# Kernel tuning notes

Hardware: AMD Instinct MI355X
Metric: run time of the kernel (lower is better)

## Reference

```python
import jax, jax.numpy as jnp
import numpy as np

HEADS = 8
KEY_DIM = 32
EPS = 1e-5


def layernorm(x, gamma, beta, eps=EPS):
    mu = jnp.mean(x, axis=-1, keepdims=True)
    var = jnp.mean(jnp.square(x - mu), axis=-1, keepdims=True)
    return (x - mu) * jax.lax.rsqrt(var + eps) * gamma + beta


def setup_inputs() -> dict:
    key = jax.random.key(0)
    ks = jax.random.split(key, 6)
    B, H, W, C = 16, 32, 32, 256
    inner = HEADS * KEY_DIM  # 256
    s = 1.0 / np.sqrt(C)
    return {
        "x": jax.random.normal(ks[0], (B, H, W, C), jnp.float32),
        "gamma": jnp.ones((C,), jnp.float32),
        "beta": jnp.zeros((C,), jnp.float32),
        "Wq": jax.random.normal(ks[1], (C, inner), jnp.float32) * s,
        "bq": jnp.zeros((inner,), jnp.float32),
        "Wk": jax.random.normal(ks[2], (C, inner), jnp.float32) * s,
        "bk": jnp.zeros((inner,), jnp.float32),
        "Wv": jax.random.normal(ks[3], (C, inner), jnp.float32) * s,
        "bv": jnp.zeros((inner,), jnp.float32),
        "Wp": jax.random.normal(ks[4], (inner, C), jnp.float32) * s,
        "bp": jnp.zeros((C,), jnp.float32),
    }


def reference(x, gamma, beta, Wq, bq, Wk, bk, Wv, bv, Wp, bp):
    B, H, W, C = x.shape
    N = H * W
    h, d = HEADS, KEY_DIM
    X = layernorm(x, gamma, beta)              # [B,H,W,C]
    Xf = X.reshape(B, N, C)                    # 1x1 conv == per-token linear
    Q = (Xf @ Wq + bq).reshape(B, N, h, d)
    K = (Xf @ Wk + bk).reshape(B, N, h, d)
    V = (Xf @ Wv + bv).reshape(B, N, h, d)
    scale = jnp.asarray(d, x.dtype) ** -0.5
    scores = jnp.einsum('bnhd,bmhd->bhnm', Q, K) * scale
    A = jax.nn.softmax(scores, axis=-1)        # [B,h,N,N]
    Y = jnp.einsum('bhnm,bmhd->bnhd', A, V).reshape(B, N, h * d)
    out = (Y @ Wp + bp).reshape(B, H, W, C)
    return out
```

## Files before the change

### kernel.cpp

```cpp
#include <hip/hip_runtime.h>
#include <hip/hip_bf16.h>

typedef __bf16 bf16_t;
typedef __attribute__((ext_vector_type(8))) __bf16 bf16x8;
typedef __attribute__((ext_vector_type(4))) float f32x4;
typedef __attribute__((ext_vector_type(4))) short s16x4;

#define GLDS16(g, l) __builtin_amdgcn_global_load_lds( \
    (const __attribute__((address_space(1))) unsigned int*)(g), \
    (__attribute__((address_space(3))) unsigned int*)(l), 16, 0, 0)

__device__ __forceinline__ float fexp2(float x) {
#if __has_builtin(__builtin_amdgcn_exp2f)
  return __builtin_amdgcn_exp2f(x);
#else
  return exp2f(x);
#endif
}

#define QSCALE (0.17677669529663688f * 1.4426950408889634f)

__global__ __launch_bounds__(256) void wtr_kernel(
    const float* __restrict__ Wq, const float* __restrict__ Wk,
    const float* __restrict__ Wv, const float* __restrict__ Wp,
    bf16_t* __restrict__ Wt)
{
  const int idx = blockIdx.x * 256 + threadIdx.x;
  const int mat = idx >> 16;
  const int e   = idx & 65535;
  const int k   = e >> 8;
  const int n   = e & 255;
  const float* W = (mat == 0) ? Wq : (mat == 1) ? Wk : (mat == 2) ? Wv : Wp;
  Wt[(size_t)mat * 65536 + n * 256 + k] = (bf16_t)W[e];
}

__global__ __launch_bounds__(256) void ln_kernel(
    const float* __restrict__ x, const float* __restrict__ gamma,
    const float* __restrict__ beta, bf16_t* __restrict__ Xln)
{
  const int wave = threadIdx.x >> 6, lane = threadIdx.x & 63;
  const int tok = blockIdx.x * 4 + wave;
  const float4 v = *reinterpret_cast<const float4*>(x + (size_t)tok * 256 + lane * 4);
  float s1 = v.x + v.y + v.z + v.w;
  float s2 = v.x*v.x + v.y*v.y + v.z*v.z + v.w*v.w;
  #pragma unroll
  for (int off = 1; off < 64; off <<= 1) {
    s1 += __shfl_xor(s1, off);
    s2 += __shfl_xor(s2, off);
  }
  const float mean = s1 * (1.0f/256.0f);
  const float var  = s2 * (1.0f/256.0f) - mean*mean;
  const float rstd = rsqrtf(var + 1e-5f);
  const float4 g  = *reinterpret_cast<const float4*>(gamma + lane*4);
  const float4 be = *reinterpret_cast<const float4*>(beta  + lane*4);
  union { bf16_t h4[4]; unsigned long long u; } pk;
  pk.h4[0] = (bf16_t)((v.x-mean)*rstd*g.x + be.x);
  pk.h4[1] = (bf16_t)((v.y-mean)*rstd*g.y + be.y);
  pk.h4[2] = (bf16_t)((v.z-mean)*rstd*g.z + be.z);
  pk.h4[3] = (bf16_t)((v.w-mean)*rstd*g.w + be.w);
  *reinterpret_cast<unsigned long long*>(Xln + (size_t)tok*256 + lane*4) = pk.u;
}

template<int MODE>
__global__ __launch_bounds__(256) void gemm_kernel(
    const bf16_t* __restrict__ A, const bf16_t* __restrict__ Wt,
    const float* __restrict__ b0, const float* __restrict__ b1,
    const float* __restrict__ b2,
    bf16_t* __restrict__ Qb, bf16_t* __restrict__ Kb, bf16_t* __restrict__ Vt,
    float* __restrict__ Fout)
{
  __shared__ __align__(16) bf16_t As[128*64];
  __shared__ __align__(16) bf16_t Bs[128*64];
  const int tid  = threadIdx.x;
  const int lane = tid & 63, wave = tid >> 6;
  const int lg = lane >> 4, li = lane & 15;
  const int wm = wave >> 1, wn = wave & 1;
  const int mt = blockIdx.x;
  const int nt = blockIdx.y;
  int mat, nbase;
  const bf16_t* Bm;
  if (MODE == 0) { mat = nt >> 1; nbase = (nt & 1) * 128; Bm = Wt + (size_t)mat * 65536; }
  else           { mat = 3;       nbase = nt * 128;       Bm = Wt; }

  f32x4 acc[4][4] = {};

  for (int kt = 0; kt < 4; ++kt) {
    __syncthreads();
    #pragma unroll
    for (int i = 0; i < 4; ++i) {
      const int idx = i*256 + tid;
      const int row = idx >> 3, ck = idx & 7;
      const int cs = ck ^ (row & 7);
      GLDS16(A + (size_t)(mt*128 + row)*256 + kt*64 + cs*8, As + idx*8);
    }
    #pragma unroll
    for (int i = 0; i < 4; ++i) {
      const int idx = i*256 + tid;
      const int row = idx >> 3, ck = idx & 7;
      const int cs = ck ^ (row & 7);
      GLDS16(Bm + (size_t)(nbase + row)*256 + kt*64 + cs*8, Bs + idx*8);
    }
    __syncthreads();
    #pragma unroll
    for (int kk = 0; kk < 2; ++kk) {
      bf16x8 af[4], bfv[4];
      #pragma unroll
      for (int mi = 0; mi < 4; ++mi) {
        const int row = wm*64 + mi*16 + li;
        const int c = (kk*4 + lg) ^ (row & 7);
        af[mi] = *reinterpret_cast<const bf16x8*>(As + row*64 + c*8);
      }
      #pragma unroll
      for (int ni = 0; ni < 4; ++ni) {
        const int row = wn*64 + ni*16 + li;
        const int c = (kk*4 + lg) ^ (row & 7);
        bfv[ni] = *reinterpret_cast<const bf16x8*>(Bs + row*64 + c*8);
      }
      #pragma unroll
      for (int mi = 0; mi < 4; ++mi)
        #pragma unroll
        for (int ni = 0; ni < 4; ++ni)
          acc[mi][ni] = __builtin_amdgcn_mfma_f32_16x16x32_bf16(af[mi], bfv[ni], acc[mi][ni], 0, 0, 0);
    }
  }

  if (MODE == 0) {
    const float* bias = (mat == 0) ? b0 : (mat == 1) ? b1 : b2;
    if (mat < 2) {
      bf16_t* Out = (mat == 0) ? Qb : Kb;
      const float osc = (mat == 0) ? QSCALE : 1.0f;
      #pragma unroll
      for (int mi = 0; mi < 4; ++mi)
        #pragma unroll
        for (int ni = 0; ni < 4; ++ni) {
          const int col = nbase + wn*64 + ni*16 + li;
          const float bb = bias[col];
          #pragma unroll
          for (int r = 0; r < 4; ++r) {
            const int row = mt*128 + wm*64 + mi*16 + lg*4 + r;
            Out[(size_t)row*256 + col] = (bf16_t)((acc[mi][ni][r] + bb) * osc);
          }
        }
    } else {
      #pragma unroll
      for (int mi = 0; mi < 4; ++mi)
        #pragma unroll
        for (int ni = 0; ni < 4; ++ni) {
          const int col = nbase + wn*64 + ni*16 + li;
          const int hh = col >> 5, dd = col & 31;
          const float bb = bias[col];
          const int row0 = mt*128 + wm*64 + mi*16 + lg*4;
          const int bi = row0 >> 10, nn = row0 & 1023;
          union { bf16_t h4[4]; unsigned long long u; } pk;
          #pragma unroll
          for (int r = 0; r < 4; ++r) pk.h4[r] = (bf16_t)(acc[mi][ni][r] + bb);
          *reinterpret_cast<unsigned long long*>(
              Vt + ((size_t)(bi*8 + hh)*32 + dd)*1024 + nn) = pk.u;
        }
    }
  } else {
    #pragma unroll
    for (int mi = 0; mi < 4; ++mi)
      #pragma unroll
      for (int ni = 0; ni < 4; ++ni) {
        const int col = nbase + wn*64 + ni*16 + li;
        const float bb = b0[col];
        #pragma unroll
        for (int r = 0; r < 4; ++r) {
          const int row = mt*128 + wm*64 + mi*16 + lg*4 + r;
          Fout[(size_t)row*256 + col] = acc[mi][ni][r] + bb;
        }
      }
  }
}

__global__ __launch_bounds__(256, 4) void attn_kernel(
    const bf16_t* __restrict__ Qb, const bf16_t* __restrict__ Kb,
    const bf16_t* __restrict__ Vt, bf16_t* __restrict__ Yb)
{
  __shared__ __align__(16) char Ks[2][4096];
  __shared__ __align__(16) char Vs[2][4096];
  const int tid  = threadIdx.x;
  const int wave = tid >> 6, lane = tid & 63;
  const int lg = lane >> 4, li = lane & 15;
  const int gid = blockIdx.x;
  const int qt = (gid >> 3) & 7;
  const int bh = ((gid >> 6) << 3) | (gid & 7);
  const int b  = bh >> 3, hh = bh & 7;
  const int tok0 = b*1024 + qt*128 + wave*32;

  const bf16x8 qf0 = *reinterpret_cast<const bf16x8*>(
      Qb + (size_t)(tok0 + li)*256 + hh*32 + lg*8);
  const bf16x8 qf1 = *reinterpret_cast<const bf16x8*>(
      Qb + (size_t)(tok0 + 16 + li)*256 + hh*32 + lg*8);

  const int kt_ = tid >> 2, ks_ = tid & 3;
  const bf16_t* Ksrc = Kb + (size_t)(b*1024 + kt_)*256 + hh*32
                          + ((ks_ ^ ((kt_ >> 1) & 3)) * 8);
  const int vd_ = tid >> 3, vs_ = tid & 7;
  const bf16_t* Vsrc = Vt + ((size_t)bh*32 + vd_)*1024
                          + ((vs_ ^ (vd_ & 7)) * 8);

  const int kof = li*64 + ((lg ^ ((li >> 1) & 3)) * 16);
  int vof[4];
  #pragma unroll
  for (int ct = 0; ct < 4; ++ct)
    vof[ct] = li*128 + (((ct*2 + (lg >> 1)) ^ (li & 7)) * 16) + (lg & 1)*8;

  const f32x4 fz = {0.f, 0.f, 0.f, 0.f};
  f32x4 acc00 = fz, acc01 = fz;
  f32x4 acc10 = fz, acc11 = fz;
  float m0 = 0.f, m1 = 0.f;
  float lrow0 = 0.f, lrow1 = 0.f;

  GLDS16(Ksrc, &Ks[0][tid*16]);
  GLDS16(Vsrc, &Vs[0][tid*16]);
  __syncthreads();

  #pragma unroll 2
  for (int mc = 0; mc < 16; ++mc) {
    const int cur = mc & 1;
    if (mc < 15) {
      GLDS16(Ksrc + (size_t)(mc+1)*16384, &Ks[cur^1][tid*16]);
      GLDS16(Vsrc + (mc+1)*64,            &Vs[cur^1][tid*16]);
    }
    const char* kb = &Ks[cur][0];
    const char* vb = &Vs[cur][0];
    f32x4 s0[4], s1[4];
    #pragma unroll
    for (int ct = 0; ct < 4; ++ct) {
      const bf16x8 kfrag = *reinterpret_cast<const bf16x8*>(kb + kof + ct*1024);
      s0[ct] = __builtin_amdgcn_mfma_f32_16x16x32_bf16(kfrag, qf0, fz, 0, 0, 0);
      s1[ct] = __builtin_amdgcn_mfma_f32_16x16x32_bf16(kfrag, qf1, fz, 0, 0, 0);
    }
    s16x4 vq0[4], vq1[4];
    #pragma unroll
    for (int ct = 0; ct < 4; ++ct) {
      vq0[ct] = *reinterpret_cast<const s16x4*>(vb + vof[ct]);
      vq1[ct] = *reinterpret_cast<const s16x4*>(vb + vof[ct] + 16*128);
    }
    {
      float mxa = fmaxf(fmaxf(s0[0][0], s0[0][1]), fmaxf(s0[0][2], s0[0][3]));
      float mxb = fmaxf(fmaxf(s0[1][0], s0[1][1]), fmaxf(s0[1][2], s0[1][3]));
      float mxc = fmaxf(fmaxf(s0[2][0], s0[2][1]), fmaxf(s0[2][2], s0[2][3]));
      float mxd = fmaxf(fmaxf(s0[3][0], s0[3][1]), fmaxf(s0[3][2], s0[3][3]));
      const float pmax = fmaxf(fmaxf(mxa, mxb), fmaxf(mxc, mxd));
      if (!__all(pmax - m0 <= 8.0f)) {
        float rmx = pmax;
        rmx = fmaxf(rmx, __shfl_xor(rmx, 16));
        rmx = fmaxf(rmx, __shfl_xor(rmx, 32));
        const float mnew = fmaxf(m0, rmx);
        const float sf = fexp2(m0 - mnew);
        lrow0 *= sf;
        #pragma unroll
        for (int r = 0; r < 4; ++r) { acc00[r] *= sf; acc01[r] *= sf; }
        m0 = mnew;
      }
      float psum = 0.f;
      #pragma unroll
      for (int ct = 0; ct < 4; ++ct) {
        #pragma unroll
        for (int r = 0; r < 4; ++r)
          s0[ct][r] = fexp2(s0[ct][r] - m0);
        psum += (s0[ct][0] + s0[ct][1]) + (s0[ct][2] + s0[ct][3]);
      }
      lrow0 += psum;
    }
    {
      float mxa = fmaxf(fmaxf(s1[0][0], s1[0][1]), fmaxf(s1[0][2], s1[0][3]));
      float mxb = fmaxf(fmaxf(s1[1][0], s1[1][1]), fmaxf(s1[1][2], s1[1][3]));
      float mxc = fmaxf(fmaxf(s1[2][0], s1[2][1]), fmaxf(s1[2][2], s1[2][3]));
      float mxd = fmaxf(fmaxf(s1[3][0], s1[3][1]), fmaxf(s1[3][2], s1[3][3]));
      const float pmax = fmaxf(fmaxf(mxa, mxb), fmaxf(mxc, mxd));
      if (!__all(pmax - m1 <= 8.0f)) {
        float rmx = pmax;
        rmx = fmaxf(rmx, __shfl_xor(rmx, 16));
        rmx = fmaxf(rmx, __shfl_xor(rmx, 32));
        const float mnew = fmaxf(m1, rmx);
        const float sf = fexp2(m1 - mnew);
        lrow1 *= sf;
        #pragma unroll
        for (int r = 0; r < 4; ++r) { acc10[r] *= sf; acc11[r] *= sf; }
        m1 = mnew;
      }
      float psum = 0.f;
      #pragma unroll
      for (int ct = 0; ct < 4; ++ct) {
        #pragma unroll
        for (int r = 0; r < 4; ++r)
          s1[ct][r] = fexp2(s1[ct][r] - m1);
        psum += (s1[ct][0] + s1[ct][1]) + (s1[ct][2] + s1[ct][3]);
      }
      lrow1 += psum;
    }
    #pragma unroll
    for (int ct = 0; ct < 4; ++ct) {
      union { bf16_t h4[4]; s16x4 v; } p0, p1;
      #pragma unroll
      for (int r = 0; r < 4; ++r) { p0.h4[r] = (bf16_t)s0[ct][r];
                                    p1.h4[r] = (bf16_t)s1[ct][r]; }
      acc00 = __builtin_amdgcn_mfma_f32_16x16x16bf16_1k(vq0[ct], p0.v, acc00, 0, 0, 0);
      acc01 = __builtin_amdgcn_mfma_f32_16x16x16bf16_1k(vq1[ct], p0.v, acc01, 0, 0, 0);
      acc10 = __builtin_amdgcn_mfma_f32_16x16x16bf16_1k(vq0[ct], p1.v, acc10, 0, 0, 0);
      acc11 = __builtin_amdgcn_mfma_f32_16x16x16bf16_1k(vq1[ct], p1.v, acc11, 0, 0, 0);
    }
    __syncthreads();
  }

  float ls0 = lrow0, ls1 = lrow1;
  ls0 += __shfl_xor(ls0, 16); ls0 += __shfl_xor(ls0, 32);
  ls1 += __shfl_xor(ls1, 16); ls1 += __shfl_xor(ls1, 32);
  const float inv0 = 1.0f / ls0, inv1 = 1.0f / ls1;
  union { bf16_t h4[4]; unsigned long long u; } o00, o01, o10, o11;
  #pragma unroll
  for (int r = 0; r < 4; ++r) {
    o00.h4[r] = (bf16_t)(acc00[r]*inv0);
    o01.h4[r] = (bf16_t)(acc01[r]*inv0);
    o10.h4[r] = (bf16_t)(acc10[r]*inv1);
    o11.h4[r] = (bf16_t)(acc11[r]*inv1);
  }
  bf16_t* yp0 = Yb + (size_t)(tok0 + li)*256 + hh*32;
  bf16_t* yp1 = Yb + (size_t)(tok0 + 16 + li)*256 + hh*32;
  *reinterpret_cast<unsigned long long*>(yp0 + lg*4)      = o00.u;
  *reinterpret_cast<unsigned long long*>(yp0 + 16 + lg*4) = o01.u;
  *reinterpret_cast<unsigned long long*>(yp1 + lg*4)      = o10.u;
  *reinterpret_cast<unsigned long long*>(yp1 + 16 + lg*4) = o11.u;
}

extern "C" void kernel_launch(void* const* d_in, const int* in_sizes, int n_in,
                              void* d_out, int out_size, void* d_ws, size_t ws_size,
                              hipStream_t stream) {
  const float* x     = (const float*)d_in[0];
  const float* gamma = (const float*)d_in[1];
  const float* beta  = (const float*)d_in[2];
  const float* Wq    = (const float*)d_in[3];
  const float* bq    = (const float*)d_in[4];
  const float* Wk    = (const float*)d_in[5];
  const float* bk    = (const float*)d_in[6];
  const float* Wv    = (const float*)d_in[7];
  const float* bv    = (const float*)d_in[8];
  const float* Wp    = (const float*)d_in[9];
  const float* bp    = (const float*)d_in[10];
  float* out = (float*)d_out;

  char* ws = (char*)d_ws;
  bf16_t* Wt  = (bf16_t*)(ws);
  bf16_t* Xln = (bf16_t*)(ws + 524288);
  bf16_t* Qb  = (bf16_t*)(ws + 8912896);
  bf16_t* Kb  = (bf16_t*)(ws + 17301504);
  bf16_t* Vt  = (bf16_t*)(ws + 25690112);
  bf16_t* Yb  = Xln;

  wtr_kernel<<<1024, 256, 0, stream>>>(Wq, Wk, Wv, Wp, Wt);
  ln_kernel<<<4096, 256, 0, stream>>>(x, gamma, beta, Xln);
  gemm_kernel<0><<<dim3(128, 6), 256, 0, stream>>>(
      Xln, Wt, bq, bk, bv, Qb, Kb, Vt, nullptr);
  attn_kernel<<<1024, 256, 0, stream>>>(Qb, Kb, Vt, Yb);
  gemm_kernel<1><<<dim3(128, 2), 256, 0, stream>>>(
      Yb, Wt + 3*65536, bp, nullptr, nullptr, nullptr, nullptr, nullptr, out);
}
```

Before: 79.42 us.

## Triple-buffer K/V tiles, compute softmax row sums via MFMA with ones

```diff
diff --git a/kernel.cpp b/kernel.cpp
--- a/kernel.cpp
+++ b/kernel.cpp
@@ -178,8 +178,8 @@
     const bf16_t* __restrict__ Qb, const bf16_t* __restrict__ Kb,
     const bf16_t* __restrict__ Vt, bf16_t* __restrict__ Yb)
 {
-  __shared__ __align__(16) char Ks[2][4096];
-  __shared__ __align__(16) char Vs[2][4096];
+  __shared__ __align__(16) char Ks[3][4096];
+  __shared__ __align__(16) char Vs[3][4096];
   const int tid  = threadIdx.x;
   const int wave = tid >> 6, lane = tid & 63;
   const int lg = lane >> 4, li = lane & 15;
@@ -210,22 +210,30 @@
   const f32x4 fz = {0.f, 0.f, 0.f, 0.f};
   f32x4 acc00 = fz, acc01 = fz;
   f32x4 acc10 = fz, acc11 = fz;
+  f32x4 accl0 = fz, accl1 = fz;
   float m0 = 0.f, m1 = 0.f;
-  float lrow0 = 0.f, lrow1 = 0.f;
-
-  GLDS16(Ksrc, &Ks[0][tid*16]);
-  GLDS16(Vsrc, &Vs[0][tid*16]);
-  __syncthreads();
-
-  #pragma unroll 2
+  bool bump0 = false, bump1 = false;
+
+  const short oneb = 0x3F80;
+  const s16x4 vone = {oneb, oneb, oneb, oneb};
+
+  GLDS16(Ksrc,         &Ks[0][tid*16]);
+  GLDS16(Vsrc,         &Vs[0][tid*16]);
+  GLDS16(Ksrc + 16384, &Ks[1][tid*16]);
+  GLDS16(Vsrc + 64,    &Vs[1][tid*16]);
+
+  #pragma unroll
   for (int mc = 0; mc < 16; ++mc) {
-    const int cur = mc & 1;
-    if (mc < 15) {
-      GLDS16(Ksrc + (size_t)(mc+1)*16384, &Ks[cur^1][tid*16]);
-      GLDS16(Vsrc + (mc+1)*64,            &Vs[cur^1][tid*16]);
-    }
-    const char* kb = &Ks[cur][0];
-    const char* vb = &Vs[cur][0];
+    if (mc < 15) asm volatile("s_waitcnt vmcnt(2)" ::: "memory");
+    else         asm volatile("s_waitcnt vmcnt(0)" ::: "memory");
+    __builtin_amdgcn_s_barrier();
+    asm volatile("" ::: "memory");
+    if (mc + 2 < 16) {
+      GLDS16(Ksrc + (size_t)(mc+2)*16384, &Ks[(mc+2)%3][tid*16]);
+      GLDS16(Vsrc + (mc+2)*64,            &Vs[(mc+2)%3][tid*16]);
+    }
+    const char* kb = &Ks[mc%3][0];
+    const char* vb = &Vs[mc%3][0];
     f32x4 s0[4], s1[4];
     #pragma unroll
     for (int ct = 0; ct < 4; ++ct) {
@@ -246,25 +254,27 @@
       float mxd = fmaxf(fmaxf(s0[3][0], s0[3][1]), fmaxf(s0[3][2], s0[3][3]));
       const float pmax = fmaxf(fmaxf(mxa, mxb), fmaxf(mxc, mxd));
       if (!__all(pmax - m0 <= 8.0f)) {
-        float rmx = pmax;
-        rmx = fmaxf(rmx, __shfl_xor(rmx, 16));
+        float rmx = fmaxf(pmax, __shfl_xor(pmax, 16));
         rmx = fmaxf(rmx, __shfl_xor(rmx, 32));
         const float mnew = fmaxf(m0, rmx);
         const float sf = fexp2(m0 - mnew);
-        lrow0 *= sf;
-        #pragma unroll
-        for (int r = 0; r < 4; ++r) { acc00[r] *= sf; acc01[r] *= sf; }
-        m0 = mnew;
-      }
-      float psum = 0.f;
-      #pragma unroll
-      for (int ct = 0; ct < 4; ++ct) {
-        #pragma unroll
-        for (int r = 0; r < 4; ++r)
-          s0[ct][r] = fexp2(s0[ct][r] - m0);
-        psum += (s0[ct][0] + s0[ct][1]) + (s0[ct][2] + s0[ct][3]);
-      }
-      lrow0 += psum;
+        #pragma unroll
+        for (int r = 0; r < 4; ++r) {
+          acc00[r] *= sf; acc01[r] *= sf; accl0[r] *= sf;
+        }
+        m0 = mnew; bump0 = true;
+      }
+      if (!bump0) {
+        #pragma unroll
+        for (int ct = 0; ct < 4; ++ct)
+          #pragma unroll
+          for (int r = 0; r < 4; ++r) s0[ct][r] = fexp2(s0[ct][r]);
+      } else {
+        #pragma unroll
+        for (int ct = 0; ct < 4; ++ct)
+          #pragma unroll
+          for (int r = 0; r < 4; ++r) s0[ct][r] = fexp2(s0[ct][r] - m0);
+      }
     }
     {
       float mxa = fmaxf(fmaxf(s1[0][0], s1[0][1]), fmaxf(s1[0][2], s1[0][3]));
@@ -273,25 +283,27 @@
       float mxd = fmaxf(fmaxf(s1[3][0], s1[3][1]), fmaxf(s1[3][2], s1[3][3]));
       const float pmax = fmaxf(fmaxf(mxa, mxb), fmaxf(mxc, mxd));
       if (!__all(pmax - m1 <= 8.0f)) {
-        float rmx = pmax;
-        rmx = fmaxf(rmx, __shfl_xor(rmx, 16));
+        float rmx = fmaxf(pmax, __shfl_xor(pmax, 16));
         rmx = fmaxf(rmx, __shfl_xor(rmx, 32));
         const float mnew = fmaxf(m1, rmx);
         const float sf = fexp2(m1 - mnew);
-        lrow1 *= sf;
-        #pragma unroll
-        for (int r = 0; r < 4; ++r) { acc10[r] *= sf; acc11[r] *= sf; }
-        m1 = mnew;
-      }
-      float psum = 0.f;
-      #pragma unroll
-      for (int ct = 0; ct < 4; ++ct) {
-        #pragma unroll
-        for (int r = 0; r < 4; ++r)
-          s1[ct][r] = fexp2(s1[ct][r] - m1);
-        psum += (s1[ct][0] + s1[ct][1]) + (s1[ct][2] + s1[ct][3]);
-      }
-      lrow1 += psum;
+        #pragma unroll
+        for (int r = 0; r < 4; ++r) {
+          acc10[r] *= sf; acc11[r] *= sf; accl1[r] *= sf;
+        }
+        m1 = mnew; bump1 = true;
+      }
+      if (!bump1) {
+        #pragma unroll
+        for (int ct = 0; ct < 4; ++ct)
+          #pragma unroll
+          for (int r = 0; r < 4; ++r) s1[ct][r] = fexp2(s1[ct][r]);
+      } else {
+        #pragma unroll
+        for (int ct = 0; ct < 4; ++ct)
+          #pragma unroll
+          for (int r = 0; r < 4; ++r) s1[ct][r] = fexp2(s1[ct][r] - m1);
+      }
     }
     #pragma unroll
     for (int ct = 0; ct < 4; ++ct) {
@@ -301,16 +313,15 @@
                                     p1.h4[r] = (bf16_t)s1[ct][r]; }
       acc00 = __builtin_amdgcn_mfma_f32_16x16x16bf16_1k(vq0[ct], p0.v, acc00, 0, 0, 0);
       acc01 = __builtin_amdgcn_mfma_f32_16x16x16bf16_1k(vq1[ct], p0.v, acc01, 0, 0, 0);
+      accl0 = __builtin_amdgcn_mfma_f32_16x16x16bf16_1k(vone,    p0.v, accl0, 0, 0, 0);
       acc10 = __builtin_amdgcn_mfma_f32_16x16x16bf16_1k(vq0[ct], p1.v, acc10, 0, 0, 0);
       acc11 = __builtin_amdgcn_mfma_f32_16x16x16bf16_1k(vq1[ct], p1.v, acc11, 0, 0, 0);
-    }
-    __syncthreads();
-  }
-
-  float ls0 = lrow0, ls1 = lrow1;
-  ls0 += __shfl_xor(ls0, 16); ls0 += __shfl_xor(ls0, 32);
-  ls1 += __shfl_xor(ls1, 16); ls1 += __shfl_xor(ls1, 32);
-  const float inv0 = 1.0f / ls0, inv1 = 1.0f / ls1;
+      accl1 = __builtin_amdgcn_mfma_f32_16x16x16bf16_1k(vone,    p1.v, accl1, 0, 0, 0);
+    }
+  }
+
+  const float inv0 = 1.0f / accl0[0];
+  const float inv1 = 1.0f / accl1[0];
   union { bf16_t h4[4]; unsigned long long u; } o00, o01, o10, o11;
   #pragma unroll
   for (int r = 0; r < 4; ++r) {
```

Result: no change. 78.28 us (-1.4%).
